# Optimization experiments

Measured on AMD Instinct MI355X. Metric: run time of the kernel, lower is better.

Reference implementation:

```python
import jax, jax.numpy as jnp
import numpy as np
from jax import lax

B, H, W, CIN = 16, 224, 224, 8
F = 256            # filter_inpt feature dim
K = 3              # ksize (square)
NC = 16            # n_channels (output channels)
NP = CIN * NC * K * K  # 1152 dynamic filter params per sample


def setup_inputs() -> dict:
    key = jax.random.key(0)
    ks = jax.random.split(key, 8)
    s_in = 1.0 / np.sqrt(F)
    return {
        "inpt": jax.random.normal(ks[0], (B, H, W, CIN), jnp.float32),
        "filter_inpt": jax.random.normal(ks[1], (B, F), jnp.float32),
        # param_layer_1 (ELU affine, F -> F)
        "W1": jax.random.normal(ks[2], (F, F), jnp.float32) * s_in,
        "b1": jnp.zeros((F,), jnp.float32),
        # dynamic_weights affine (F -> NP), uniform_unit_scaling(0.1)-like scale
        "Wd": jax.random.normal(ks[3], (F, NP), jnp.float32) * (0.1 * s_in),
        "bd": jnp.zeros((NP,), jnp.float32),
        # dynamic_bias affine (F -> NC), scale sqrt(2)
        "Wb": jax.random.normal(ks[4], (F, NC), jnp.float32) * (np.sqrt(2.0) * s_in),
        "bb": jnp.zeros((NC,), jnp.float32),
        # static learned bias (1,1,1,NC)
        "dfn_bias": jax.random.normal(ks[5], (1, 1, 1, NC), jnp.float32) * 0.01,
    }


def reference(inpt, filter_inpt, W1, b1, Wd, bd, Wb, bb, dfn_bias):
    # param layers: (n_param_layers - 1) = 1 ELU affine keeping width F
    h = jax.nn.elu(filter_inpt @ W1 + b1)                      # [B, F]
    dyn = h @ Wd + bd                                          # [B, CIN*NC*K*K]
    # per-sample filter, ordered (Cin, kh, kw, out_ch) to match patch layout below
    w = dyn.reshape(B, CIN * K * K, NC)                        # [B, P, NC]
    # im2col patches: conv_general_dilated_patches on NCHW -> [B, CIN*K*K, H, W]
    patches = lax.conv_general_dilated_patches(
        jnp.transpose(inpt, (0, 3, 1, 2)), (K, K), (1, 1), 'SAME')
    patches = jnp.transpose(patches, (0, 2, 3, 1))             # [B, H, W, P]
    out = jnp.einsum('bhwp,bpc->bhwc', patches, w)             # [B, H, W, NC]
    # adaptive (per-sample) bias + static bias
    out = out + (h @ Wb + bb)[:, None, None, :] + dfn_bias
    return jax.nn.elu(out)
```

## Files before the change

kernel.cpp:

```cpp
#include <hip/hip_runtime.h>
#include <math.h>

constexpr int BN  = 16;
constexpr int HH  = 224;
constexpr int WW  = 224;
constexpr int CI  = 8;
constexpr int FF  = 256;
constexpr int NC  = 16;
constexpr int NP  = 1152;

typedef __attribute__((ext_vector_type(8))) short short8;
typedef __attribute__((ext_vector_type(4))) float f32x4;

__device__ __forceinline__ float elu_f(float x) {
    return x > 0.0f ? x : (__expf(x) - 1.0f);
}

__device__ __forceinline__ void split8(const float* v, short8& hi, short8& lo) {
#pragma unroll
    for (int j = 0; j < 8; ++j) {
        const unsigned u = __float_as_uint(v[j]);
        hi[j] = (short)(u >> 16);
        const float hf = __uint_as_float(u & 0xffff0000u);
        lo[j] = (short)(__float_as_uint(v[j] - hf) >> 16);
    }
}

__global__ __launch_bounds__(128) void k_h(const float* __restrict__ fi,
                                           const float* __restrict__ W1,
                                           const float* __restrict__ b1,
                                           const float* __restrict__ bd,
                                           const float* __restrict__ bb,
                                           const float* __restrict__ dfn,
                                           float* __restrict__ hp,
                                           float* __restrict__ w_out,
                                           float* __restrict__ bias_out) {
    __shared__ float x[64];
    const int bid  = blockIdx.x;
    const int b    = bid >> 3;
    const int half = (bid >> 2) & 1;
    const int ks   = bid & 3;
    const int t    = threadIdx.x;

    if (t < 64) x[t] = fi[b * FF + ks * 64 + t];
    __syncthreads();

    const int col = half * 128 + t;
    float acc = (ks == 0) ? b1[col] : 0.0f;
#pragma unroll 8
    for (int k = 0; k < 64; ++k)
        acc = fmaf(x[k], W1[(ks * 64 + k) * FF + col], acc);
    hp[(ks * BN + b) * FF + col] = acc;

    const int gid = bid * 128 + t;
    for (int i = gid; i < BN * NP; i += 16384) {
        const int c = i - (i / NP) * NP;
        w_out[i] = bd[c];
    }
    if (gid < BN * NC) bias_out[gid] = bb[gid & 15] + dfn[gid & 15];
}

__global__ __launch_bounds__(128) void k_dyn(const float* __restrict__ hp,
                                             const float* __restrict__ Wd,
                                             const float* __restrict__ Wb,
                                             float* __restrict__ w_out,
                                             float* __restrict__ bias_out) {
    __shared__ float hs[16][32];
    const int bid = blockIdx.x;
    const int cg  = bid % 9;
    const int ks  = bid / 9;
    const int k0  = ks * 32;
    const int t   = threadIdx.x;

#pragma unroll
    for (int j = 0; j < 4; ++j) {
        const int idx = t + 128 * j;
        const int bi = idx >> 5, kk = idx & 31;
        const int o = bi * FF + k0 + kk;
        const float s = hp[o] + hp[BN * FF + o] +
                        hp[2 * BN * FF + o] + hp[3 * BN * FF + o];
        hs[bi][kk] = elu_f(s);
    }
    __syncthreads();

    const int i = cg * 128 + t;
    float a[16];
#pragma unroll
    for (int b = 0; b < 16; ++b) a[b] = 0.0f;

#pragma unroll 8
    for (int kk = 0; kk < 32; ++kk) {
        const float w = Wd[(size_t)(k0 + kk) * NP + i];
#pragma unroll
        for (int b = 0; b < 16; ++b) a[b] = fmaf(hs[b][kk], w, a[b]);
    }
#pragma unroll
    for (int b = 0; b < 16; ++b) atomicAdd(&w_out[b * NP + i], a[b]);

    if (cg == 0) {
#pragma unroll
        for (int r = 0; r < 2; ++r) {
            const int p = t + r * 128;
            const int b = p >> 4, c = p & 15;
            float s = 0.0f;
#pragma unroll 8
            for (int kk = 0; kk < 32; ++kk)
                s = fmaf(hs[b][kk], Wb[(size_t)(k0 + kk) * NC + c], s);
            atomicAdd(&bias_out[b * NC + c], s);
        }
    }
}

__global__ __launch_bounds__(128) void k_conv(const float* __restrict__ in,
                                              const float* __restrict__ w_all,
                                              const float* __restrict__ bias_all,
                                              float* __restrict__ out) {
    __shared__ short8 lsA[4][116][2];

    const int b    = blockIdx.z;
    const int half = blockIdx.x;
    const int t    = threadIdx.x;
    const int wid  = t >> 6;
    const int lane = t & 63;
    const int cl   = lane & 15;
    const int g    = lane >> 4;
    const int yb0  = blockIdx.y * 2;
    const int xb0  = half * 112;

    for (int s = t; s < 456; s += 128) {
        const int r  = s / 114;
        const int j  = s - r * 114;
        const int gy = yb0 - 1 + r;
        const int gx = xb0 - 1 + j;
        const bool ok = ((unsigned)gy < (unsigned)HH) &&
                        ((unsigned)gx < (unsigned)WW);
        float av[8] = {0.f, 0.f, 0.f, 0.f, 0.f, 0.f, 0.f, 0.f};
        if (ok) {
            const float4* pp =
                (const float4*)(in + ((size_t)(b * HH + gy) * WW + gx) * CI);
            const float4 a0 = pp[0];
            const float4 a1 = pp[1];
            av[0] = a0.x; av[1] = a0.y; av[2] = a0.z; av[3] = a0.w;
            av[4] = a1.x; av[5] = a1.y; av[6] = a1.z; av[7] = a1.w;
        }
        short8 hi, lo;
        split8(av, hi, lo);
        lsA[r][j][0] = hi;
        lsA[r][j][1] = lo;
    }

    int  dyL[3], dxL[3];
    bool real[3];
#pragma unroll
    for (int c = 0; c < 3; ++c) {
        const int tap = c * 4 + g;
        real[c] = (tap < 9);
        const int tp = real[c] ? tap : 0;
        dyL[c] = tp / 3;
        dxL[c] = tp - 3 * dyL[c];
    }

    const float* __restrict__ wq = w_all + b * NP;
    short8 bhi0, blo0, bhi1, blo1, bhi2, blo2;
    {
        float wv[8];
#pragma unroll
        for (int i = 0; i < 8; ++i)
            wv[i] = real[0] ? wq[(i * 9 + (0 * 4 + g)) * NC + cl] : 0.0f;
        split8(wv, bhi0, blo0);
#pragma unroll
        for (int i = 0; i < 8; ++i)
            wv[i] = real[1] ? wq[(i * 9 + (1 * 4 + g)) * NC + cl] : 0.0f;
        split8(wv, bhi1, blo1);
#pragma unroll
        for (int i = 0; i < 8; ++i)
            wv[i] = real[2] ? wq[(i * 9 + (2 * 4 + g)) * NC + cl] : 0.0f;
        split8(wv, bhi2, blo2);
    }

    __syncthreads();

    const float4 bias4 = ((const float4*)(bias_all + b * NC))[g];
    const int y = yb0 + wid;
    const size_t orow = ((size_t)(b * HH + y) * WW) * NC;

#pragma unroll 1
    for (int tx = 0; tx < 7; ++tx) {
        const int x0 = xb0 + tx * 16;
        f32x4 accM = {bias4.x, bias4.y, bias4.z, bias4.w};
        f32x4 accL = {0.f, 0.f, 0.f, 0.f};
        f32x4 accH = {0.f, 0.f, 0.f, 0.f};

#pragma unroll
        for (int c = 0; c < 3; ++c) {
            const int j = tx * 16 + cl + dxL[c];
            const int r = wid + dyL[c];
            const short8 ahi = lsA[r][j][0];
            const short8 alo = lsA[r][j][1];
            const short8 bh = (c == 0) ? bhi0 : (c == 1) ? bhi1 : bhi2;
            const short8 bl = (c == 0) ? blo0 : (c == 1) ? blo1 : blo2;
            accM = __builtin_amdgcn_mfma_f32_16x16x32_bf16(bh, ahi, accM, 0, 0, 0);
            accL = __builtin_amdgcn_mfma_f32_16x16x32_bf16(bh, alo, accL, 0, 0, 0);
            accH = __builtin_amdgcn_mfma_f32_16x16x32_bf16(bl, ahi, accH, 0, 0, 0);
        }

        float4 res;
        res.x = elu_f(accM[0] + accL[0] + accH[0]);
        res.y = elu_f(accM[1] + accL[1] + accH[1]);
        res.z = elu_f(accM[2] + accL[2] + accH[2]);
        res.w = elu_f(accM[3] + accL[3] + accH[3]);
        ((float4*)(out + orow + (size_t)(x0 + cl) * NC))[g] = res;
    }
}

extern "C" void kernel_launch(void* const* d_in, const int* in_sizes, int n_in,
                              void* d_out, int out_size, void* d_ws, size_t ws_size,
                              hipStream_t stream) {
    const float* inpt = (const float*)d_in[0];
    const float* fi   = (const float*)d_in[1];
    const float* W1   = (const float*)d_in[2];
    const float* b1   = (const float*)d_in[3];
    const float* Wd   = (const float*)d_in[4];
    const float* bd   = (const float*)d_in[5];
    const float* Wb   = (const float*)d_in[6];
    const float* bb   = (const float*)d_in[7];
    const float* dfn  = (const float*)d_in[8];
    float* out = (float*)d_out;

    float* ws    = (float*)d_ws;
    float* hp    = ws;
    float* wDyn  = ws + 16384;
    float* biasA = ws + 16384 + 18432;

    k_h  <<<128, 128, 0, stream>>>(fi, W1, b1, bd, bb, dfn, hp, wDyn, biasA);
    k_dyn<<<72, 128, 0, stream>>>(hp, Wd, Wb, wDyn, biasA);
    k_conv<<<dim3(2, 112, BN), 128, 0, stream>>>(inpt, wDyn, biasA, out);
}
```

Baseline: 39.73 us.

## Replace atomic split-K reduction in dynamic-weight GEMV with partial buffers reduced in conv

The dynamic weight kernel now launches one block per sample, column group and K-slice, 576 blocks instead of 72. Each block writes its partial sums to a separate buffer instead of atomically adding into a pre-initialized output. The conv kernel sums the four partials plus the static biases when it loads its filter and bias values. This removes the atomics and the bias-initialization pass in k_h and spreads the GEMV across more blocks. In exchange, every conv block performs extra global reads, five loads per weight element, and Wd is re-read once per sample.

```diff
diff --git a/kernel.cpp b/kernel.cpp
--- a/kernel.cpp
+++ b/kernel.cpp
@@ -29,12 +29,7 @@
 __global__ __launch_bounds__(128) void k_h(const float* __restrict__ fi,
                                            const float* __restrict__ W1,
                                            const float* __restrict__ b1,
-                                           const float* __restrict__ bd,
-                                           const float* __restrict__ bb,
-                                           const float* __restrict__ dfn,
-                                           float* __restrict__ hp,
-                                           float* __restrict__ w_out,
-                                           float* __restrict__ bias_out) {
+                                           float* __restrict__ hp) {
     __shared__ float x[64];
     const int bid  = blockIdx.x;
     const int b    = bid >> 3;
@@ -51,69 +46,52 @@
     for (int k = 0; k < 64; ++k)
         acc = fmaf(x[k], W1[(ks * 64 + k) * FF + col], acc);
     hp[(ks * BN + b) * FF + col] = acc;
-
-    const int gid = bid * 128 + t;
-    for (int i = gid; i < BN * NP; i += 16384) {
-        const int c = i - (i / NP) * NP;
-        w_out[i] = bd[c];
-    }
-    if (gid < BN * NC) bias_out[gid] = bb[gid & 15] + dfn[gid & 15];
 }
 
 __global__ __launch_bounds__(128) void k_dyn(const float* __restrict__ hp,
                                              const float* __restrict__ Wd,
                                              const float* __restrict__ Wb,
-                                             float* __restrict__ w_out,
-                                             float* __restrict__ bias_out) {
-    __shared__ float hs[16][32];
+                                             float* __restrict__ wPart,
+                                             float* __restrict__ biasPart) {
+    __shared__ float hs[64];
     const int bid = blockIdx.x;
-    const int cg  = bid % 9;
-    const int ks  = bid / 9;
-    const int k0  = ks * 32;
+    const int b   = bid / 36;
+    const int r   = bid - b * 36;
+    const int cg  = r >> 2;
+    const int ks  = r & 3;
+    const int k0  = ks * 64;
     const int t   = threadIdx.x;
 
-#pragma unroll
-    for (int j = 0; j < 4; ++j) {
-        const int idx = t + 128 * j;
-        const int bi = idx >> 5, kk = idx & 31;
-        const int o = bi * FF + k0 + kk;
+    if (t < 64) {
+        const int o = b * FF + k0 + t;
         const float s = hp[o] + hp[BN * FF + o] +
                         hp[2 * BN * FF + o] + hp[3 * BN * FF + o];
-        hs[bi][kk] = elu_f(s);
+        hs[t] = elu_f(s);
     }
     __syncthreads();
 
     const int i = cg * 128 + t;
-    float a[16];
-#pragma unroll
-    for (int b = 0; b < 16; ++b) a[b] = 0.0f;
-
+    float acc = 0.0f;
 #pragma unroll 8
-    for (int kk = 0; kk < 32; ++kk) {
-        const float w = Wd[(size_t)(k0 + kk) * NP + i];
-#pragma unroll
-        for (int b = 0; b < 16; ++b) a[b] = fmaf(hs[b][kk], w, a[b]);
-    }
-#pragma unroll
-    for (int b = 0; b < 16; ++b) atomicAdd(&w_out[b * NP + i], a[b]);
-
-    if (cg == 0) {
-#pragma unroll
-        for (int r = 0; r < 2; ++r) {
-            const int p = t + r * 128;
-            const int b = p >> 4, c = p & 15;
-            float s = 0.0f;
+    for (int kk = 0; kk < 64; ++kk)
+        acc = fmaf(hs[kk], Wd[(size_t)(k0 + kk) * NP + i], acc);
+    wPart[(size_t)ks * BN * NP + b * NP + i] = acc;
+
+    if (cg == 0 && t < NC) {
+        float s = 0.0f;
 #pragma unroll 8
-            for (int kk = 0; kk < 32; ++kk)
-                s = fmaf(hs[b][kk], Wb[(size_t)(k0 + kk) * NC + c], s);
-            atomicAdd(&bias_out[b * NC + c], s);
-        }
+        for (int kk = 0; kk < 64; ++kk)
+            s = fmaf(hs[kk], Wb[(size_t)(k0 + kk) * NC + t], s);
+        biasPart[ks * BN * NC + b * NC + t] = s;
     }
 }
 
 __global__ __launch_bounds__(128) void k_conv(const float* __restrict__ in,
-                                              const float* __restrict__ w_all,
-                                              const float* __restrict__ bias_all,
+                                              const float* __restrict__ wPart,
+                                              const float* __restrict__ biasPart,
+                                              const float* __restrict__ bd,
+                                              const float* __restrict__ bb,
+                                              const float* __restrict__ dfn,
                                               float* __restrict__ out) {
     __shared__ short8 lsA[4][116][2];
 
@@ -160,34 +138,56 @@
         dxL[c] = tp - 3 * dyL[c];
     }
 
-    const float* __restrict__ wq = w_all + b * NP;
+    const float* __restrict__ wp0 = wPart + (size_t)b * NP;
     short8 bhi0, blo0, bhi1, blo1, bhi2, blo2;
     {
         float wv[8];
 #pragma unroll
-        for (int i = 0; i < 8; ++i)
-            wv[i] = real[0] ? wq[(i * 9 + (0 * 4 + g)) * NC + cl] : 0.0f;
+        for (int i = 0; i < 8; ++i) {
+            const int idx = (i * 9 + (0 * 4 + g)) * NC + cl;
+            wv[i] = real[0] ? (bd[idx] + wp0[idx] + wp0[BN * NP + idx] +
+                               wp0[2 * BN * NP + idx] + wp0[3 * BN * NP + idx])
+                            : 0.0f;
+        }
         split8(wv, bhi0, blo0);
 #pragma unroll
-        for (int i = 0; i < 8; ++i)
-            wv[i] = real[1] ? wq[(i * 9 + (1 * 4 + g)) * NC + cl] : 0.0f;
+        for (int i = 0; i < 8; ++i) {
+            const int idx = (i * 9 + (1 * 4 + g)) * NC + cl;
+            wv[i] = real[1] ? (bd[idx] + wp0[idx] + wp0[BN * NP + idx] +
+                               wp0[2 * BN * NP + idx] + wp0[3 * BN * NP + idx])
+                            : 0.0f;
+        }
         split8(wv, bhi1, blo1);
 #pragma unroll
-        for (int i = 0; i < 8; ++i)
-            wv[i] = real[2] ? wq[(i * 9 + (2 * 4 + g)) * NC + cl] : 0.0f;
+        for (int i = 0; i < 8; ++i) {
+            const int idx = (i * 9 + (2 * 4 + g)) * NC + cl;
+            wv[i] = real[2] ? (bd[idx] + wp0[idx] + wp0[BN * NP + idx] +
+                               wp0[2 * BN * NP + idx] + wp0[3 * BN * NP + idx])
+                            : 0.0f;
+        }
         split8(wv, bhi2, blo2);
     }
 
+    float bias_v[4];
+#pragma unroll
+    for (int j = 0; j < 4; ++j) {
+        const int ch = g * 4 + j;
+        bias_v[j] = bb[ch] + dfn[ch] +
+                    biasPart[0 * BN * NC + b * NC + ch] +
+                    biasPart[1 * BN * NC + b * NC + ch] +
+                    biasPart[2 * BN * NC + b * NC + ch] +
+                    biasPart[3 * BN * NC + b * NC + ch];
+    }
+
     __syncthreads();
 
-    const float4 bias4 = ((const float4*)(bias_all + b * NC))[g];
     const int y = yb0 + wid;
     const size_t orow = ((size_t)(b * HH + y) * WW) * NC;
 
 #pragma unroll 1
     for (int tx = 0; tx < 7; ++tx) {
         const int x0 = xb0 + tx * 16;
-        f32x4 accM = {bias4.x, bias4.y, bias4.z, bias4.w};
+        f32x4 accM = {bias_v[0], bias_v[1], bias_v[2], bias_v[3]};
         f32x4 accL = {0.f, 0.f, 0.f, 0.f};
         f32x4 accH = {0.f, 0.f, 0.f, 0.f};
 
@@ -227,12 +227,13 @@
     const float* dfn  = (const float*)d_in[8];
     float* out = (float*)d_out;
 
-    float* ws    = (float*)d_ws;
-    float* hp    = ws;
-    float* wDyn  = ws + 16384;
-    float* biasA = ws + 16384 + 18432;
-
-    k_h  <<<128, 128, 0, stream>>>(fi, W1, b1, bd, bb, dfn, hp, wDyn, biasA);
-    k_dyn<<<72, 128, 0, stream>>>(hp, Wd, Wb, wDyn, biasA);
-    k_conv<<<dim3(2, 112, BN), 128, 0, stream>>>(inpt, wDyn, biasA, out);
-}
+    float* ws       = (float*)d_ws;
+    float* hp       = ws;
+    float* wPart    = ws + 16384;
+    float* biasPart = ws + 16384 + 73728;
+
+    k_h  <<<128, 128, 0, stream>>>(fi, W1, b1, hp);
+    k_dyn<<<576, 128, 0, stream>>>(hp, Wd, Wb, wPart, biasPart);
+    k_conv<<<dim3(2, 112, BN), 128, 0, stream>>>(inpt, wPart, biasPart,
+                                                 bd, bb, dfn, out);
+}
```

New measurement: 46.19 us. 16.2% more time.

## Fuse hidden-layer and dynamic-weight kernels into one launch without atomics

Applied to the files above, without the earlier changes.

Merges the hidden-layer kernel and the dynamic-filter kernel into a single kernel where each block recomputes the full ELU hidden vector for its sample and then produces a 128-column slice of dynamic weights plus the adaptive bias. This removes one kernel launch, the partial-sum workspace and all atomicAdd accumulation, and initializes biases inline. The tradeoff is redundant recomputation of the W1 product in each of the 9 column blocks per sample and longer serial reduction loops per thread.

```diff
diff --git a/kernel.cpp b/kernel.cpp
--- a/kernel.cpp
+++ b/kernel.cpp
@@ -26,88 +26,58 @@
     }
 }
 
-__global__ __launch_bounds__(128) void k_h(const float* __restrict__ fi,
-                                           const float* __restrict__ W1,
-                                           const float* __restrict__ b1,
-                                           const float* __restrict__ bd,
-                                           const float* __restrict__ bb,
-                                           const float* __restrict__ dfn,
-                                           float* __restrict__ hp,
-                                           float* __restrict__ w_out,
-                                           float* __restrict__ bias_out) {
-    __shared__ float x[64];
-    const int bid  = blockIdx.x;
-    const int b    = bid >> 3;
-    const int half = (bid >> 2) & 1;
-    const int ks   = bid & 3;
-    const int t    = threadIdx.x;
-
-    if (t < 64) x[t] = fi[b * FF + ks * 64 + t];
+__global__ __launch_bounds__(128) void k_hdyn(const float* __restrict__ fi,
+                                              const float* __restrict__ W1,
+                                              const float* __restrict__ b1,
+                                              const float* __restrict__ Wd,
+                                              const float* __restrict__ bd,
+                                              const float* __restrict__ Wb,
+                                              const float* __restrict__ bb,
+                                              const float* __restrict__ dfn,
+                                              float* __restrict__ w_all,
+                                              float* __restrict__ bias_all) {
+    __shared__ float fis[FF];
+    __shared__ float hs[FF];
+    const int cg = blockIdx.x;
+    const int b  = blockIdx.y;
+    const int t  = threadIdx.x;
+
+    fis[t]       = fi[b * FF + t];
+    fis[t + 128] = fi[b * FF + t + 128];
     __syncthreads();
 
-    const int col = half * 128 + t;
-    float acc = (ks == 0) ? b1[col] : 0.0f;
+    {
+        float a0 = b1[t],       a1 = 0.0f;
+        float c0 = b1[t + 128], c1 = 0.0f;
 #pragma unroll 8
-    for (int k = 0; k < 64; ++k)
-        acc = fmaf(x[k], W1[(ks * 64 + k) * FF + col], acc);
-    hp[(ks * BN + b) * FF + col] = acc;
-
-    const int gid = bid * 128 + t;
-    for (int i = gid; i < BN * NP; i += 16384) {
-        const int c = i - (i / NP) * NP;
-        w_out[i] = bd[c];
-    }
-    if (gid < BN * NC) bias_out[gid] = bb[gid & 15] + dfn[gid & 15];
-}
-
-__global__ __launch_bounds__(128) void k_dyn(const float* __restrict__ hp,
-                                             const float* __restrict__ Wd,
-                                             const float* __restrict__ Wb,
-                                             float* __restrict__ w_out,
-                                             float* __restrict__ bias_out) {
-    __shared__ float hs[16][32];
-    const int bid = blockIdx.x;
-    const int cg  = bid % 9;
-    const int ks  = bid / 9;
-    const int k0  = ks * 32;
-    const int t   = threadIdx.x;
-
-#pragma unroll
-    for (int j = 0; j < 4; ++j) {
-        const int idx = t + 128 * j;
-        const int bi = idx >> 5, kk = idx & 31;
-        const int o = bi * FF + k0 + kk;
-        const float s = hp[o] + hp[BN * FF + o] +
-                        hp[2 * BN * FF + o] + hp[3 * BN * FF + o];
-        hs[bi][kk] = elu_f(s);
+        for (int k = 0; k < 128; ++k) {
+            a0 = fmaf(fis[k],       W1[k * FF + t],               a0);
+            c0 = fmaf(fis[k],       W1[k * FF + t + 128],         c0);
+            a1 = fmaf(fis[k + 128], W1[(k + 128) * FF + t],       a1);
+            c1 = fmaf(fis[k + 128], W1[(k + 128) * FF + t + 128], c1);
+        }
+        hs[t]       = elu_f(a0 + a1);
+        hs[t + 128] = elu_f(c0 + c1);
     }
     __syncthreads();
 
     const int i = cg * 128 + t;
-    float a[16];
-#pragma unroll
-    for (int b = 0; b < 16; ++b) a[b] = 0.0f;
-
+    float a0 = bd[i], a1 = 0.0f;
 #pragma unroll 8
-    for (int kk = 0; kk < 32; ++kk) {
-        const float w = Wd[(size_t)(k0 + kk) * NP + i];
-#pragma unroll
-        for (int b = 0; b < 16; ++b) a[b] = fmaf(hs[b][kk], w, a[b]);
-    }
-#pragma unroll
-    for (int b = 0; b < 16; ++b) atomicAdd(&w_out[b * NP + i], a[b]);
-
-    if (cg == 0) {
-#pragma unroll
-        for (int r = 0; r < 2; ++r) {
-            const int p = t + r * 128;
-            const int b = p >> 4, c = p & 15;
-            float s = 0.0f;
+    for (int k = 0; k < 128; ++k) {
+        a0 = fmaf(hs[k],       Wd[(size_t)k * NP + i],         a0);
+        a1 = fmaf(hs[k + 128], Wd[(size_t)(k + 128) * NP + i], a1);
+    }
+    w_all[b * NP + i] = a0 + a1;
+
+    if (cg == 0 && t < NC) {
+        float s0 = bb[t] + dfn[t], s1 = 0.0f;
 #pragma unroll 8
-            for (int kk = 0; kk < 32; ++kk)
-                s = fmaf(hs[b][kk], Wb[(size_t)(k0 + kk) * NC + c], s);
-            atomicAdd(&bias_out[b * NC + c], s);
-        }
+        for (int k = 0; k < 128; ++k) {
+            s0 = fmaf(hs[k],       Wb[k * NC + t],         s0);
+            s1 = fmaf(hs[k + 128], Wb[(k + 128) * NC + t], s1);
+        }
+        bias_all[b * NC + t] = s0 + s1;
     }
 }
 
@@ -228,11 +198,10 @@
     float* out = (float*)d_out;
 
     float* ws    = (float*)d_ws;
-    float* hp    = ws;
-    float* wDyn  = ws + 16384;
-    float* biasA = ws + 16384 + 18432;
-
-    k_h  <<<128, 128, 0, stream>>>(fi, W1, b1, bd, bb, dfn, hp, wDyn, biasA);
-    k_dyn<<<72, 128, 0, stream>>>(hp, Wd, Wb, wDyn, biasA);
+    float* wDyn  = ws;
+    float* biasA = ws + 18432;
+
+    k_hdyn<<<dim3(9, BN), 128, 0, stream>>>(fi, W1, b1, Wd, bd, Wb, bb, dfn,
+                                            wDyn, biasA);
     k_conv<<<dim3(2, 112, BN), 128, 0, stream>>>(inpt, wDyn, biasA, out);
 }
```

After: 47.49 us. +19.5%, slower.
